# Kernel optimization log

Hardware: AMD Instinct MI355X
Metric: run time of the kernel (lower is better)

The kernel has to match this reference:

```python
import jax, jax.numpy as jnp
import numpy as np

# DeepNovo config constants
MASS_H2O = 18.01056
MASS_NH3 = 17.02655
MS_RESOLUTION = 10.0          # bins per Dalton
WINDOW_SIZE = 10
MAX_MZ = 30000                # 3000 Da * 10 bins/Da
_PAD, _GO, _EOS = 0, 1, 2
VOCAB = 26
BATCH = 32768


def setup_inputs() -> dict:
    key = jax.random.key(0)
    k1, k2, k3, k4 = jax.random.split(key, 4)
    spectrum = jax.random.uniform(k1, (MAX_MZ,), dtype=jnp.float32)
    pepmass = jax.random.uniform(k2, (BATCH,), dtype=jnp.float32, minval=500.0, maxval=2500.0)
    prefix_mass = jax.random.uniform(k3, (BATCH,), dtype=jnp.float32) * pepmass * 0.8
    # amino-acid residue masses roughly in [57, 186] Da
    masses = jax.random.uniform(k4, (VOCAB,), dtype=jnp.float32, minval=57.0, maxval=186.0)
    return {"spectrum": spectrum, "pepmass": pepmass, "prefix_mass": prefix_mass,
            "masses": masses, "direction": 0}


def reference(spectrum, pepmass, prefix_mass, masses, direction):
    if direction == 0:
        first_label, last_label = _GO, _EOS
        cb = prefix_mass[:, None] + masses[None, :]      # [B, V]
        cy = pepmass[:, None] - cb
    else:
        first_label, last_label = _EOS, _GO
        cy = prefix_mass[:, None] + masses[None, :]
        cb = pepmass[:, None] - cy
    # 8 ion types: b, b-H2O, b-NH3, b++, y, y-H2O, y-NH3, y++  -> [B, V, 8]
    ion_mass = jnp.stack([cb, cb - MASS_H2O, cb - MASS_NH3, cb / 2,
                          cy, cy - MASS_H2O, cy - MASS_NH3, cy / 2], axis=-1)
    inf_idx = jnp.round(ion_mass * MS_RESOLUTION).astype(jnp.int32) - WINDOW_SIZE // 2
    valid = (inf_idx >= 0) & (inf_idx <= MAX_MZ - WINDOW_SIZE)   # [B, V, 8]
    safe = jnp.where(valid, inf_idx, 0)
    slices = safe[..., None] + jnp.arange(WINDOW_SIZE, dtype=jnp.int32)  # [B, V, 8, W]
    gathered = jnp.take(spectrum, slices) * valid[..., None].astype(spectrum.dtype)
    # zero out FIRST/LAST/PAD vocab rows (for both directions the set is {_PAD,_GO,_EOS})
    label_mask = jnp.ones((VOCAB,), spectrum.dtype).at[
        jnp.array([_PAD, first_label, last_label])].set(0.0)
    return gathered * label_mask[None, :, None, None]
```

## Files before the change

### kernel.cpp

```cpp
#include <hip/hip_runtime.h>
#include <hip/hip_fp16.h>


#define MASS_H2O 18.01056f
#define MASS_NH3 17.02655f

constexpr int MAX_MZ = 30000;
constexpr int WIN = 10;
constexpr int VOCAB = 26;
constexpr int BLOCK = 512;
constexpr int GRID = 512;

__global__ __launch_bounds__(BLOCK, 4) void intensity_kernel(
    const float* __restrict__ spectrum,
    const float* __restrict__ pepmass,
    const float* __restrict__ prefix_mass,
    const float* __restrict__ masses,
    const int*   __restrict__ dir_p,
    float* __restrict__ out,
    int n_vec4)
{
    __shared__ __half sspec[MAX_MZ];

    {
        const float2* sp2 = reinterpret_cast<const float2*>(spectrum);
        __half2* dst = reinterpret_cast<__half2*>(sspec);
        for (int i = threadIdx.x; i < MAX_MZ / 2; i += BLOCK) {
            float2 v = sp2[i];
            dst[i] = __floats2half2_rn(v.x, v.y);
        }
    }
    __syncthreads();

    const int dir = dir_p[0];
    const int stride = GRID * BLOCK;

    for (int tid = blockIdx.x * BLOCK + threadIdx.x; tid < n_vec4; tid += stride) {
        int g = tid / 20;
        int q = tid - g * 20;
        int b = g / VOCAB;
        int v = g - b * VOCAB;

        float pm = pepmass[b];
        float pf = prefix_mass[b];
        float ms = masses[v];

        float t = pf + ms;
        float u = pm - t;
        float cb = (dir == 0) ? t : u;
        float cy = (dir == 0) ? u : t;

        float lmask = (v > 2) ? 1.0f : 0.0f;

        float vals[4];
#pragma unroll
        for (int j = 0; j < 4; ++j) {
            int e   = 4 * q + j;
            int ion = e / WIN;
            int w   = e - ion * WIN;

            float m = (ion < 4) ? cb : cy;
            int k = ion & 3;
            m = (k == 1) ? (m - MASS_H2O)
              : (k == 2) ? (m - MASS_NH3)
              : (k == 3) ? (m * 0.5f)
              : m;

            int idx = (int)rintf(m * 10.0f) - (WIN / 2);
            bool valid = (idx >= 0) && (idx <= MAX_MZ - WIN);
            int safe = valid ? idx : 0;
            float s = __half2float(sspec[safe + w]);
            vals[j] = valid ? (s * lmask) : 0.0f;
        }

        float4 r;
        r.x = vals[0]; r.y = vals[1]; r.z = vals[2]; r.w = vals[3];
        reinterpret_cast<float4*>(out)[tid] = r;
    }
}

extern "C" void kernel_launch(void* const* d_in, const int* in_sizes, int n_in,
                              void* d_out, int out_size, void* d_ws, size_t ws_size,
                              hipStream_t stream) {
    const float* spectrum    = (const float*)d_in[0];
    const float* pepmass     = (const float*)d_in[1];
    const float* prefix_mass = (const float*)d_in[2];
    const float* masses      = (const float*)d_in[3];
    const int*   direction   = (const int*)d_in[4];
    float* out = (float*)d_out;

    int n_vec4 = out_size / 4;
    intensity_kernel<<<GRID, BLOCK, 0, stream>>>(
        spectrum, pepmass, prefix_mass, masses, direction, out, n_vec4);
}
```

Before: 308.2 us.

## Map each block to whole batch rows and hoist per-thread ion constants

Thread-to-output mapping is restructured so each block handles one batch row per iteration, with 520 active threads each owning a fixed (vocab, quad) slot. This removes the per-element integer divisions, lets mass, label mask and ion offset/scale be computed once per thread, and collapses the ion-type selects into an add and a multiply. Block size grows to 640, so 120 threads per block sit idle after the shared-memory fill, and the launch bound changes to 5 blocks per CU. Batch size is now taken from the input size instead of the output size.

```diff
diff --git a/kernel.cpp b/kernel.cpp
--- a/kernel.cpp
+++ b/kernel.cpp
@@ -8,17 +8,18 @@
 constexpr int MAX_MZ = 30000;
 constexpr int WIN = 10;
 constexpr int VOCAB = 26;
-constexpr int BLOCK = 512;
-constexpr int GRID = 512;
+constexpr int BLOCK = 640;
+constexpr int GRID  = 512;
+constexpr int CPB   = VOCAB * 20;
 
-__global__ __launch_bounds__(BLOCK, 4) void intensity_kernel(
+__global__ __launch_bounds__(BLOCK, 5) void intensity_kernel(
     const float* __restrict__ spectrum,
     const float* __restrict__ pepmass,
     const float* __restrict__ prefix_mass,
     const float* __restrict__ masses,
     const int*   __restrict__ dir_p,
     float* __restrict__ out,
-    int n_vec4)
+    int batch)
 {
     __shared__ __half sspec[MAX_MZ];
 
@@ -26,56 +27,64 @@
         const float2* sp2 = reinterpret_cast<const float2*>(spectrum);
         __half2* dst = reinterpret_cast<__half2*>(sspec);
         for (int i = threadIdx.x; i < MAX_MZ / 2; i += BLOCK) {
-            float2 v = sp2[i];
-            dst[i] = __floats2half2_rn(v.x, v.y);
+            float2 t = sp2[i];
+            dst[i] = __floats2half2_rn(t.x, t.y);
         }
     }
     __syncthreads();
 
+    const int c = threadIdx.x;
+    if (c >= CPB) return;
+
     const int dir = dir_p[0];
-    const int stride = GRID * BLOCK;
 
-    for (int tid = blockIdx.x * BLOCK + threadIdx.x; tid < n_vec4; tid += stride) {
-        int g = tid / 20;
-        int q = tid - g * 20;
-        int b = g / VOCAB;
-        int v = g - b * VOCAB;
+    const int v = c / 20;
+    const int q = c - v * 20;
+    const float ms = masses[v];
+    const float lmask = (v > 2) ? 1.0f : 0.0f;
 
+    bool  selcy[4];
+    float addj[4];
+    float mulj[4];
+    int   wj[4];
+#pragma unroll
+    for (int j = 0; j < 4; ++j) {
+        int e = 4 * q + j;
+        int ion = e / 10;
+        wj[j] = e - ion * 10;
+        selcy[j] = (ion >= 4);
+        int k = ion & 3;
+        addj[j] = (k == 1) ? -MASS_H2O : (k == 2) ? -MASS_NH3 : 0.0f;
+        mulj[j] = (k == 3) ? 0.5f : 1.0f;
+    }
+
+    float4* op = reinterpret_cast<float4*>(out) + (size_t)blockIdx.x * CPB + c;
+    const size_t ostride = (size_t)GRID * CPB;
+
+    for (int b = blockIdx.x; b < batch; b += GRID) {
         float pm = pepmass[b];
         float pf = prefix_mass[b];
-        float ms = masses[v];
-
         float t = pf + ms;
         float u = pm - t;
         float cb = (dir == 0) ? t : u;
         float cy = (dir == 0) ? u : t;
 
-        float lmask = (v > 2) ? 1.0f : 0.0f;
-
         float vals[4];
 #pragma unroll
         for (int j = 0; j < 4; ++j) {
-            int e   = 4 * q + j;
-            int ion = e / WIN;
-            int w   = e - ion * WIN;
-
-            float m = (ion < 4) ? cb : cy;
-            int k = ion & 3;
-            m = (k == 1) ? (m - MASS_H2O)
-              : (k == 2) ? (m - MASS_NH3)
-              : (k == 3) ? (m * 0.5f)
-              : m;
-
+            float base = selcy[j] ? cy : cb;
+            float m = (base + addj[j]) * mulj[j];
             int idx = (int)rintf(m * 10.0f) - (WIN / 2);
-            bool valid = (idx >= 0) && (idx <= MAX_MZ - WIN);
+            bool valid = (unsigned)idx <= (unsigned)(MAX_MZ - WIN);
             int safe = valid ? idx : 0;
-            float s = __half2float(sspec[safe + w]);
-            vals[j] = valid ? (s * lmask) : 0.0f;
+            float s = __half2float(sspec[safe + wj[j]]);
+            vals[j] = valid ? s * lmask : 0.0f;
         }
 
         float4 r;
         r.x = vals[0]; r.y = vals[1]; r.z = vals[2]; r.w = vals[3];
-        reinterpret_cast<float4*>(out)[tid] = r;
+        *op = r;
+        op += ostride;
     }
 }
 
@@ -89,7 +98,7 @@
     const int*   direction   = (const int*)d_in[4];
     float* out = (float*)d_out;
 
-    int n_vec4 = out_size / 4;
+    int batch = in_sizes[1];
     intensity_kernel<<<GRID, BLOCK, 0, stream>>>(
-        spectrum, pepmass, prefix_mass, masses, direction, out, n_vec4);
+        spectrum, pepmass, prefix_mass, masses, direction, out, batch);
 }
```

New measurement: 323.4 us. 4.9% more time.
